# Performance work log

Measured on AMD Instinct MI355X. Metric: run time of the kernel, lower is better.

The kernel has to match this reference:

```python
import jax, jax.numpy as jnp
import numpy as np

B, C, H, W = 4, 256, 64, 64
D = C // 8  # query/key projection dim


def setup_inputs() -> dict:
    key = jax.random.key(0)
    ks = jax.random.split(key, 8)
    s = 0.02
    return {
        "x": jax.random.normal(ks[0], (B, C, H, W), dtype=jnp.float32),
        "Wq": jax.random.normal(ks[1], (D, C), dtype=jnp.float32) * s,
        "bq": jax.random.normal(ks[2], (D,), dtype=jnp.float32) * s,
        "Wk": jax.random.normal(ks[3], (D, C), dtype=jnp.float32) * s,
        "bk": jax.random.normal(ks[4], (D,), dtype=jnp.float32) * s,
        "Wv": jax.random.normal(ks[5], (C, C), dtype=jnp.float32) * s,
        "bv": jax.random.normal(ks[6], (C,), dtype=jnp.float32) * s,
        "gamma": jax.random.normal(ks[7], (1,), dtype=jnp.float32),
    }


def reference(x, Wq, bq, Wk, bk, Wv, bv, gamma):
    b, c, h, w = x.shape
    n = h * w
    xf = x.reshape(b, c, n)                                  # B,C,N
    # 1x1 convs == per-pixel linear projections
    q = jnp.einsum("dc,bcn->bdn", Wq, xf) + bq[None, :, None]  # B,D,N
    k = jnp.einsum("dc,bcn->bdn", Wk, xf) + bk[None, :, None]  # B,D,N
    v = jnp.einsum("ec,bcn->ben", Wv, xf) + bv[None, :, None]  # B,C,N
    # energy[b,i,j] = <q[:, i], k[:, j]>  (query index i, key index j)
    energy = jnp.einsum("bdi,bdj->bij", q, k)                # B,N,N
    attention = jax.nn.softmax(energy, axis=-1)              # softmax over keys j
    # out[b,c,i] = sum_j v[b,c,j] * attention[b,i,j]
    out = jnp.einsum("bcj,bij->bci", v, attention)           # B,C,N
    out = out.reshape(b, c, h, w)
    return gamma[0] * out + x
```

## Files before the change

kernel.cpp:

```cpp
#include <hip/hip_runtime.h>
#include <hip/hip_bf16.h>
#include <cstdint>

#define B_ 4
#define C_ 256
#define N_ 4096
#define D_ 32
#define LOG2E 1.44269504088896f

typedef __attribute__((ext_vector_type(8))) short bf16x8;
typedef __attribute__((ext_vector_type(4))) short s16x4;
typedef __attribute__((ext_vector_type(4))) float f32x4;
typedef __attribute__((ext_vector_type(4))) int i32x4;

__device__ inline unsigned short f2bf(float f) {
    union { float f; uint32_t u; } v; v.f = f;
    uint32_t u = v.u;
    u += 0x7FFFu + ((u >> 16) & 1u);
    return (unsigned short)(u >> 16);
}

__device__ inline float exp2_raw(float x) {
    float r;
    asm("v_exp_f32 %0, %1" : "=v"(r) : "v"(x));
    return r;
}

__global__ __launch_bounds__(256) void wconv_kernel(
    const float* __restrict__ Wq, const float* __restrict__ Wk,
    const float* __restrict__ Wv, unsigned short* __restrict__ Wb)
{
    int i = (blockIdx.x * 256 + threadIdx.x) * 4;
    int r = i >> 8, k = i & 255;
    const float* src = (r < 32) ? Wq + r * 256 + k
                     : (r < 64) ? Wk + (r - 32) * 256 + k
                                : Wv + (r - 64) * 256 + k;
    f32x4 v = *reinterpret_cast<const f32x4*>(src);
    s16x4 o;
    #pragma unroll
    for (int j = 0; j < 4; ++j) o[j] = (short)f2bf(v[j]);
    *reinterpret_cast<s16x4*>(Wb + i) = o;
}

__global__ __launch_bounds__(256) void proj_kernel(
    const float* __restrict__ x, const unsigned short* __restrict__ Wb,
    const float* __restrict__ bq, const float* __restrict__ bk,
    const float* __restrict__ bv,
    unsigned short* __restrict__ Qt, unsigned short* __restrict__ Kt,
    unsigned short* __restrict__ V)
{
    __shared__ __align__(16) char smem[16384];
    const int t  = threadIdx.x;
    const int w  = t >> 6;
    const int l  = t & 63;
    const int lg = l >> 4;
    const int ll = l & 15;
    const int n0 = blockIdx.x * 32;
    const int b  = blockIdx.y;

    #pragma unroll
    for (int rep = 0; rep < 8; ++rep) {
        int flat = rep * 256 + t;
        int c = flat >> 3, chunk = flat & 7;
        f32x4 xv = *reinterpret_cast<const f32x4*>(
            x + ((size_t)(b * C_ + c)) * N_ + n0 + chunk * 4);
        #pragma unroll
        for (int j = 0; j < 4; ++j) {
            int n = chunk * 4 + j;
            *reinterpret_cast<unsigned short*>(
                smem + n * 512 + ((c * 2) ^ ((n & 7) << 4))) = f2bf(xv[j]);
        }
    }

    bf16x8 Af[5], Afn[5];
    #pragma unroll
    for (int rt = 0; rt < 5; ++rt) {
        int r = w * 80 + rt * 16 + ll;
        Af[rt] = *reinterpret_cast<const bf16x8*>(Wb + r * 256 + lg * 8);
    }

    f32x4 acc[5][2];
    #pragma unroll
    for (int rt = 0; rt < 5; ++rt)
        #pragma unroll
        for (int nt = 0; nt < 2; ++nt) acc[rt][nt] = (f32x4){0.f, 0.f, 0.f, 0.f};

    __syncthreads();

    for (int kc = 0; kc < 8; ++kc) {
        const int kcn = (kc + 1) & 7;
        #pragma unroll
        for (int rt = 0; rt < 5; ++rt) {
            int r = w * 80 + rt * 16 + ll;
            Afn[rt] = *reinterpret_cast<const bf16x8*>(
                Wb + r * 256 + kcn * 32 + lg * 8);
        }
        bf16x8 Bf[2];
        #pragma unroll
        for (int nt = 0; nt < 2; ++nt) {
            int n = nt * 16 + ll;
            Bf[nt] = *reinterpret_cast<const bf16x8*>(
                smem + n * 512 + ((kc * 64 + lg * 16) ^ ((n & 7) << 4)));
        }
        #pragma unroll
        for (int rt = 0; rt < 5; ++rt)
            #pragma unroll
            for (int nt = 0; nt < 2; ++nt)
                acc[rt][nt] = __builtin_amdgcn_mfma_f32_16x16x32_bf16(
                    Af[rt], Bf[nt], acc[rt][nt], 0, 0, 0);
        #pragma unroll
        for (int rt = 0; rt < 5; ++rt) Af[rt] = Afn[rt];
    }

    #pragma unroll
    for (int rt = 0; rt < 5; ++rt) {
        const int rrow = w * 80 + rt * 16 + lg * 4;
        float bias[4];
        #pragma unroll
        for (int q = 0; q < 4; ++q) {
            int rg = rrow + q;
            bias[q] = (rg < 32) ? bq[rg] : (rg < 64) ? bk[rg - 32] : bv[rg - 64];
        }
        if (rrow < 64) {
            const int d0 = rrow & 31;
            const bool isQ = (rrow < 32);
            unsigned short* dst = isQ ? Qt : Kt;
            #pragma unroll
            for (int nt = 0; nt < 2; ++nt) {
                int n = n0 + nt * 16 + ll;
                s16x4 sv;
                #pragma unroll
                for (int q = 0; q < 4; ++q) {
                    float v = acc[rt][nt][q] + bias[q];
                    if (isQ) v *= LOG2E;
                    sv[q] = (short)f2bf(v);
                }
                *reinterpret_cast<s16x4*>(dst + ((size_t)b * N_ + n) * D_ + d0) = sv;
            }
        } else {
            #pragma unroll
            for (int nt = 0; nt < 2; ++nt) {
                int n = n0 + nt * 16 + ll;
                #pragma unroll
                for (int q = 0; q < 4; ++q) {
                    int c = rrow - 64 + q;
                    V[((size_t)(b * C_ + c)) * N_ + n] = f2bf(acc[rt][nt][q] + bias[q]);
                }
            }
        }
    }
}

__global__ __launch_bounds__(512) void attn_kernel(
    const unsigned short* __restrict__ Qt, const unsigned short* __restrict__ Kt,
    const unsigned short* __restrict__ Vg, const float* __restrict__ x,
    const float* __restrict__ gamma, float* __restrict__ out)
{
    __shared__ __align__(16) char smem[41472];
    char* Pbase = smem + 32768;
    float* LbufF = reinterpret_cast<float*>(smem + 40960);
    const int t  = threadIdx.x;
    const int w  = t >> 6;
    const int l  = t & 63;
    const int lg = l >> 4;
    const int ll = l & 15;
    const int qt_p = w >> 2;
    const int jc   = w & 3;
    const int bid  = blockIdx.x;
    const int id   = (bid & 7) * 64 + (bid >> 3);
    const int b    = id >> 7;
    const int n0   = (id & 127) * 32;

    const unsigned short* vsrc[4];
    int vdst[4];
    #pragma unroll
    for (int i = 0; i < 4; ++i) {
        int Lb  = i * 8192 + w * 1024 + l * 16;
        int c   = Lb >> 7;
        int off = Lb & 127;
        vsrc[i] = Vg + ((size_t)(b * C_ + c)) * N_ + (off >> 1);
        vdst[i] = c * 128 + (off ^ ((c & 7) << 4));
    }

    const bf16x8 qfrag = *reinterpret_cast<const bf16x8*>(
        Qt + ((size_t)b * N_ + n0 + qt_p * 16 + ll) * D_ + 8 * lg);

    f32x4 acc[2][2];
    #pragma unroll
    for (int qt = 0; qt < 2; ++qt)
        #pragma unroll
        for (int ct = 0; ct < 2; ++ct) acc[qt][ct] = (f32x4){0.f, 0.f, 0.f, 0.f};
    float l_lane[4] = {0.f, 0.f, 0.f, 0.f};

    i32x4 vr[4];
    #pragma unroll
    for (int i = 0; i < 4; ++i) vr[i] = *reinterpret_cast<const i32x4*>(vsrc[i]);
    #pragma unroll
    for (int i = 0; i < 4; ++i) *reinterpret_cast<i32x4*>(smem + vdst[i]) = vr[i];
    #pragma unroll
    for (int i = 0; i < 4; ++i) vr[i] = *reinterpret_cast<const i32x4*>(vsrc[i] + 64);

    bf16x8 kcur = *reinterpret_cast<const bf16x8*>(
        Kt + ((size_t)b * N_ + jc * 16 + ll) * D_ + 8 * lg);

    asm volatile("s_waitcnt lgkmcnt(0)" ::: "memory");
    __builtin_amdgcn_s_barrier();
    asm volatile("" ::: "memory");

    const f32x4 zero4 = {0.f, 0.f, 0.f, 0.f};

    for (int kt = 0; kt < 64; ++kt) {
        const int pb  = kt & 1;
        const int ktn = (kt < 63) ? kt + 1 : 63;

        bf16x8 knxt = *reinterpret_cast<const bf16x8*>(
            Kt + ((size_t)b * N_ + ktn * 64 + jc * 16 + ll) * D_ + 8 * lg);

        f32x4 sf = __builtin_amdgcn_mfma_f32_16x16x32_bf16(qfrag, kcur, zero4, 0, 0, 0);

        float pv[4];
        #pragma unroll
        for (int r = 0; r < 4; ++r) {
            float p = exp2_raw(fminf(sf[r], 86.f));
            pv[r] = p;
            l_lane[r] += p;
        }

        char* Pw = Pbase + pb * 4096;
        #pragma unroll
        for (int r = 0; r < 4; ++r) {
            int row = qt_p * 16 + lg * 4 + r;
            int col = jc * 16 + ll;
            *reinterpret_cast<unsigned short*>(
                Pw + row * 128 + ((col * 2) ^ ((row & 7) << 4))) = f2bf(pv[r]);
        }

        asm volatile("s_waitcnt lgkmcnt(0)" ::: "memory");
        __builtin_amdgcn_s_barrier();
        asm volatile("" ::: "memory");

        char* Pr = Pbase + pb * 4096;
        bf16x8 pfrag[2][2];
        #pragma unroll
        for (int qt = 0; qt < 2; ++qt)
            #pragma unroll
            for (int kh = 0; kh < 2; ++kh) {
                int row = qt * 16 + ll;
                pfrag[qt][kh] = *reinterpret_cast<const bf16x8*>(
                    Pr + row * 128 + ((kh * 64 + lg * 16) ^ ((row & 7) << 4)));
            }
        __builtin_amdgcn_s_setprio(1);
        #pragma unroll
        for (int ct = 0; ct < 2; ++ct) {
            int cl = w * 32 + ct * 16 + ll;
            #pragma unroll
            for (int kh = 0; kh < 2; ++kh) {
                bf16x8 vf = *reinterpret_cast<const bf16x8*>(
                    smem + cl * 128 + ((kh * 64 + lg * 16) ^ ((cl & 7) << 4)));
                #pragma unroll
                for (int qt = 0; qt < 2; ++qt)
                    acc[qt][ct] = __builtin_amdgcn_mfma_f32_16x16x32_bf16(
                        pfrag[qt][kh], vf, acc[qt][ct], 0, 0, 0);
            }
        }
        __builtin_amdgcn_s_setprio(0);

        asm volatile("s_waitcnt lgkmcnt(0)" ::: "memory");
        __builtin_amdgcn_s_barrier();
        asm volatile("" ::: "memory");

        if (kt < 63) {
            #pragma unroll
            for (int i = 0; i < 4; ++i)
                *reinterpret_cast<i32x4*>(smem + vdst[i]) = vr[i];
            if (kt < 62) {
                #pragma unroll
                for (int i = 0; i < 4; ++i)
                    vr[i] = *reinterpret_cast<const i32x4*>(vsrc[i] + (kt + 2) * 64);
            }
        }

        kcur = knxt;
    }

    #pragma unroll
    for (int off = 1; off < 16; off <<= 1)
        #pragma unroll
        for (int r = 0; r < 4; ++r)
            l_lane[r] += __shfl_xor(l_lane[r], off);
    if (ll == 0) {
        #pragma unroll
        for (int r = 0; r < 4; ++r) LbufF[w * 16 + lg * 4 + r] = l_lane[r];
    }
    __syncthreads();

    float inv[2][4];
    #pragma unroll
    for (int qt = 0; qt < 2; ++qt)
        #pragma unroll
        for (int r = 0; r < 4; ++r) {
            int lq = lg * 4 + r;
            float ls = LbufF[(qt * 4 + 0) * 16 + lq] + LbufF[(qt * 4 + 1) * 16 + lq]
                     + LbufF[(qt * 4 + 2) * 16 + lq] + LbufF[(qt * 4 + 3) * 16 + lq];
            inv[qt][r] = 1.f / ls;
        }

    #pragma unroll
    for (int qt = 0; qt < 2; ++qt)
        #pragma unroll
        for (int ct = 0; ct < 2; ++ct) {
            int cl = w * 32 + ct * 16 + ll;
            int ncol = qt * 16 + lg * 4;
            f32x4 v;
            #pragma unroll
            for (int r = 0; r < 4; ++r) v[r] = acc[qt][ct][r] * inv[qt][r];
            *reinterpret_cast<f32x4*>(smem + cl * 128 + ((ncol * 4) ^ ((cl & 7) << 4))) = v;
        }
    __syncthreads();

    const float g0 = gamma[0];
    #pragma unroll
    for (int p = 0; p < 4; ++p) {
        int li = p * 512 + t;
        int cl = li >> 3;
        int n4 = (li & 7) * 4;
        f32x4 ov = *reinterpret_cast<const f32x4*>(
            smem + cl * 128 + ((n4 * 4) ^ ((cl & 7) << 4)));
        size_t gi = ((size_t)(b * C_ + cl)) * N_ + n0 + n4;
        f32x4 xv = *reinterpret_cast<const f32x4*>(x + gi);
        f32x4 res;
        #pragma unroll
        for (int j = 0; j < 4; ++j) res[j] = g0 * ov[j] + xv[j];
        *reinterpret_cast<f32x4*>(out + gi) = res;
    }
}

extern "C" void kernel_launch(void* const* d_in, const int* in_sizes, int n_in,
                              void* d_out, int out_size, void* d_ws, size_t ws_size,
                              hipStream_t stream) {
    const float* x     = (const float*)d_in[0];
    const float* Wq    = (const float*)d_in[1];
    const float* bq    = (const float*)d_in[2];
    const float* Wk    = (const float*)d_in[3];
    const float* bk    = (const float*)d_in[4];
    const float* Wv    = (const float*)d_in[5];
    const float* bv    = (const float*)d_in[6];
    const float* gamma = (const float*)d_in[7];
    float* out = (float*)d_out;

    char* ws = (char*)d_ws;
    unsigned short* Qt = (unsigned short*)(ws);
    unsigned short* Kt = (unsigned short*)(ws + (1u << 20));
    unsigned short* V  = (unsigned short*)(ws + (2u << 20));
    unsigned short* Wb = (unsigned short*)(ws + (10u << 20));

    wconv_kernel<<<dim3(80), 256, 0, stream>>>(Wq, Wk, Wv, Wb);
    proj_kernel<<<dim3(N_ / 32, B_), 256, 0, stream>>>(
        x, Wb, bq, bk, bv, Qt, Kt, V);
    attn_kernel<<<dim3(512), 512, 0, stream>>>(
        Qt, Kt, V, x, gamma, out);
}
```

Baseline: 170.6 us.

## Load V fragments directly from global memory instead of staging through LDS

The attention kernel stops staging each 64-key V tile through shared memory with a register double buffer and an extra barrier per iteration. Each wave now loads its own V MFMA operands straight from global (L2) memory, which shrinks LDS from about 41KB to 8.7KB and removes one block barrier per key tile. The epilogue writes results directly from the accumulators instead of transposing through LDS. In exchange, global load latency sits on the critical path without an explicit prefetch, and the output stores become less coalesced.

Result: slower. 227.2 us (+33.2%).

```diff
diff --git a/kernel.cpp b/kernel.cpp
--- a/kernel.cpp
+++ b/kernel.cpp
@@ -11,7 +11,6 @@
 typedef __attribute__((ext_vector_type(8))) short bf16x8;
 typedef __attribute__((ext_vector_type(4))) short s16x4;
 typedef __attribute__((ext_vector_type(4))) float f32x4;
-typedef __attribute__((ext_vector_type(4))) int i32x4;
 
 __device__ inline unsigned short f2bf(float f) {
     union { float f; uint32_t u; } v; v.f = f;
@@ -156,9 +155,9 @@
     const unsigned short* __restrict__ Vg, const float* __restrict__ x,
     const float* __restrict__ gamma, float* __restrict__ out)
 {
-    __shared__ __align__(16) char smem[41472];
-    char* Pbase = smem + 32768;
-    float* LbufF = reinterpret_cast<float*>(smem + 40960);
+    __shared__ __align__(16) char smem[8704];
+    char* Pbase = smem;
+    float* LbufF = reinterpret_cast<float*>(smem + 8192);
     const int t  = threadIdx.x;
     const int w  = t >> 6;
     const int l  = t & 63;
@@ -171,20 +170,12 @@
     const int b    = id >> 7;
     const int n0   = (id & 127) * 32;
 
-    const unsigned short* vsrc[4];
-    int vdst[4];
-    #pragma unroll
-    for (int i = 0; i < 4; ++i) {
-        int Lb  = i * 8192 + w * 1024 + l * 16;
-        int c   = Lb >> 7;
-        int off = Lb & 127;
-        vsrc[i] = Vg + ((size_t)(b * C_ + c)) * N_ + (off >> 1);
-        vdst[i] = c * 128 + (off ^ ((c & 7) << 4));
-    }
-
     const bf16x8 qfrag = *reinterpret_cast<const bf16x8*>(
         Qt + ((size_t)b * N_ + n0 + qt_p * 16 + ll) * D_ + 8 * lg);
 
+    const unsigned short* vbase =
+        Vg + ((size_t)(b * C_ + w * 32 + ll)) * N_ + lg * 8;
+
     f32x4 acc[2][2];
     #pragma unroll
     for (int qt = 0; qt < 2; ++qt)
@@ -192,26 +183,22 @@
         for (int ct = 0; ct < 2; ++ct) acc[qt][ct] = (f32x4){0.f, 0.f, 0.f, 0.f};
     float l_lane[4] = {0.f, 0.f, 0.f, 0.f};
 
-    i32x4 vr[4];
-    #pragma unroll
-    for (int i = 0; i < 4; ++i) vr[i] = *reinterpret_cast<const i32x4*>(vsrc[i]);
-    #pragma unroll
-    for (int i = 0; i < 4; ++i) *reinterpret_cast<i32x4*>(smem + vdst[i]) = vr[i];
-    #pragma unroll
-    for (int i = 0; i < 4; ++i) vr[i] = *reinterpret_cast<const i32x4*>(vsrc[i] + 64);
-
     bf16x8 kcur = *reinterpret_cast<const bf16x8*>(
         Kt + ((size_t)b * N_ + jc * 16 + ll) * D_ + 8 * lg);
-
-    asm volatile("s_waitcnt lgkmcnt(0)" ::: "memory");
-    __builtin_amdgcn_s_barrier();
-    asm volatile("" ::: "memory");
 
     const f32x4 zero4 = {0.f, 0.f, 0.f, 0.f};
 
     for (int kt = 0; kt < 64; ++kt) {
         const int pb  = kt & 1;
         const int ktn = (kt < 63) ? kt + 1 : 63;
+
+        bf16x8 vf[2][2];
+        #pragma unroll
+        for (int ct = 0; ct < 2; ++ct)
+            #pragma unroll
+            for (int kh = 0; kh < 2; ++kh)
+                vf[ct][kh] = *reinterpret_cast<const bf16x8*>(
+                    vbase + (size_t)(ct * 16) * N_ + kt * 64 + kh * 32);
 
         bf16x8 knxt = *reinterpret_cast<const bf16x8*>(
             Kt + ((size_t)b * N_ + ktn * 64 + jc * 16 + ll) * D_ + 8 * lg);
@@ -251,34 +238,14 @@
             }
         __builtin_amdgcn_s_setprio(1);
         #pragma unroll
-        for (int ct = 0; ct < 2; ++ct) {
-            int cl = w * 32 + ct * 16 + ll;
-            #pragma unroll
-            for (int kh = 0; kh < 2; ++kh) {
-                bf16x8 vf = *reinterpret_cast<const bf16x8*>(
-                    smem + cl * 128 + ((kh * 64 + lg * 16) ^ ((cl & 7) << 4)));
+        for (int ct = 0; ct < 2; ++ct)
+            #pragma unroll
+            for (int kh = 0; kh < 2; ++kh)
                 #pragma unroll
                 for (int qt = 0; qt < 2; ++qt)
                     acc[qt][ct] = __builtin_amdgcn_mfma_f32_16x16x32_bf16(
-                        pfrag[qt][kh], vf, acc[qt][ct], 0, 0, 0);
-            }
-        }
+                        pfrag[qt][kh], vf[ct][kh], acc[qt][ct], 0, 0, 0);
         __builtin_amdgcn_s_setprio(0);
-
-        asm volatile("s_waitcnt lgkmcnt(0)" ::: "memory");
-        __builtin_amdgcn_s_barrier();
-        asm volatile("" ::: "memory");
-
-        if (kt < 63) {
-            #pragma unroll
-            for (int i = 0; i < 4; ++i)
-                *reinterpret_cast<i32x4*>(smem + vdst[i]) = vr[i];
-            if (kt < 62) {
-                #pragma unroll
-                for (int i = 0; i < 4; ++i)
-                    vr[i] = *reinterpret_cast<const i32x4*>(vsrc[i] + (kt + 2) * 64);
-            }
-        }
 
         kcur = knxt;
     }
@@ -305,34 +272,20 @@
             inv[qt][r] = 1.f / ls;
         }
 
+    const float g0 = gamma[0];
     #pragma unroll
     for (int qt = 0; qt < 2; ++qt)
         #pragma unroll
         for (int ct = 0; ct < 2; ++ct) {
             int cl = w * 32 + ct * 16 + ll;
-            int ncol = qt * 16 + lg * 4;
-            f32x4 v;
-            #pragma unroll
-            for (int r = 0; r < 4; ++r) v[r] = acc[qt][ct][r] * inv[qt][r];
-            *reinterpret_cast<f32x4*>(smem + cl * 128 + ((ncol * 4) ^ ((cl & 7) << 4))) = v;
-        }
-    __syncthreads();
-
-    const float g0 = gamma[0];
-    #pragma unroll
-    for (int p = 0; p < 4; ++p) {
-        int li = p * 512 + t;
-        int cl = li >> 3;
-        int n4 = (li & 7) * 4;
-        f32x4 ov = *reinterpret_cast<const f32x4*>(
-            smem + cl * 128 + ((n4 * 4) ^ ((cl & 7) << 4)));
-        size_t gi = ((size_t)(b * C_ + cl)) * N_ + n0 + n4;
-        f32x4 xv = *reinterpret_cast<const f32x4*>(x + gi);
-        f32x4 res;
-        #pragma unroll
-        for (int j = 0; j < 4; ++j) res[j] = g0 * ov[j] + xv[j];
-        *reinterpret_cast<f32x4*>(out + gi) = res;
-    }
+            size_t gi = ((size_t)(b * C_ + cl)) * N_ + n0 + qt * 16 + lg * 4;
+            f32x4 xv = *reinterpret_cast<const f32x4*>(x + gi);
+            f32x4 res;
+            #pragma unroll
+            for (int r = 0; r < 4; ++r)
+                res[r] = g0 * (acc[qt][ct][r] * inv[qt][r]) + xv[r];
+            *reinterpret_cast<f32x4*>(out + gi) = res;
+        }
 }
 
 extern "C" void kernel_launch(void* const* d_in, const int* in_sizes, int n_in,
```
